# Kernel optimization log

Measured on AMD Instinct MI355X. Metric: run time of the kernel, lower is better.

## Reference

```python
import jax, jax.numpy as jnp
import numpy as np

IDIM, CDIM, NUM_HEADS, N, M = 256, 512, 2, 128, 64
T, BSZ = 64, 128


def setup_inputs() -> dict:
    key = jax.random.key(0)
    ks = jax.random.split(key, 12)
    return {
        "embs": jax.random.normal(ks[0], (T, BSZ, IDIM), jnp.float32),
        "lens": jnp.clip(jax.random.randint(ks[1], (BSZ,), 0, 64), 1, T).astype(jnp.int32),
        "mem_bias": jax.random.normal(ks[2], (N, M), jnp.float32) * 0.05,
        "W_ih": jax.random.normal(ks[3], (4 * CDIM, IDIM + NUM_HEADS * M), jnp.float32) * 0.04,
        "W_hh": jax.random.normal(ks[4], (4 * CDIM, CDIM), jnp.float32) * 0.04,
        "b_ih": jnp.zeros((4 * CDIM,), jnp.float32),
        "b_hh": jnp.zeros((4 * CDIM,), jnp.float32),
        "Wr": jax.random.normal(ks[5], (NUM_HEADS, M + 6, CDIM), jnp.float32) * 0.04,
        "br": jnp.zeros((NUM_HEADS, M + 6), jnp.float32),
        "Ww": jax.random.normal(ks[6], (NUM_HEADS, 3 * M + 6, CDIM), jnp.float32) * 0.04,
        "bw": jnp.zeros((NUM_HEADS, 3 * M + 6), jnp.float32),
        "h0": jax.random.normal(ks[7], (CDIM,), jnp.float32) * 0.05,
        "c0": jax.random.normal(ks[8], (CDIM,), jnp.float32) * 0.05,
        "r0": jax.random.normal(ks[9], (NUM_HEADS, M), jnp.float32) * 0.02,
    }


def _address(mem, k, beta, g, s, gamma, w_prev):
    # mem: (b,N,M)  k:(b,M)  beta,g,gamma:(b,1)  s:(b,3)  w_prev:(b,N)
    beta = jax.nn.softplus(beta)
    g = jax.nn.sigmoid(g)
    s = jax.nn.softmax(s, axis=1)
    gamma = 1.0 + jax.nn.softplus(gamma)
    kk = k + 1e-16
    mm = mem + 1e-16
    dot = jnp.einsum('bnm,bm->bn', mm, kk)
    denom = jnp.linalg.norm(mm, axis=-1) * jnp.linalg.norm(kk, axis=-1, keepdims=True)
    sim = dot / jnp.maximum(denom, 1e-8)  # torch cosine_similarity eps
    wc = jax.nn.softmax(beta * sim, axis=1)
    wg = g * wc + (1.0 - g) * w_prev
    # circular convolution with 3-tap shift kernel: c[i]=s0*w[i-1]+s1*w[i]+s2*w[i+1]
    ww = (s[:, 0:1] * jnp.roll(wg, 1, axis=1)
          + s[:, 1:2] * wg
          + s[:, 2:3] * jnp.roll(wg, -1, axis=1))
    wp = ww ** gamma
    return wp / (jnp.sum(wp, axis=1, keepdims=True) + 1e-16)


def _split5(o):
    return o[:, :M], o[:, M:M + 1], o[:, M + 1:M + 2], o[:, M + 2:M + 5], o[:, M + 5:M + 6]


def _ntm_forward(embs, mem_bias, W_ih, W_hh, b_ih, b_hh, Wr, br, Ww, bw, h0, c0, r0):
    bsz = embs.shape[1]
    mem0 = jnp.broadcast_to(mem_bias, (bsz, N, M))
    reads0 = jnp.broadcast_to(r0[:, None, :], (NUM_HEADS, bsz, M))
    w0 = jnp.zeros((NUM_HEADS, bsz, N), embs.dtype)
    h = jnp.broadcast_to(h0, (bsz, CDIM))
    c = jnp.broadcast_to(c0, (bsz, CDIM))

    def step(carry, emb):
        h, c, mem, rw, wws, reads = carry
        x = jnp.concatenate([emb] + [reads[i] for i in range(NUM_HEADS)], axis=1)
        gates = x @ W_ih.T + h @ W_hh.T + (b_ih + b_hh)
        gi, gf, gg, go = jnp.split(gates, 4, axis=1)  # torch LSTM gate order i,f,g,o
        c = jax.nn.sigmoid(gf) * c + jax.nn.sigmoid(gi) * jnp.tanh(gg)
        h = jax.nn.sigmoid(go) * jnp.tanh(c)
        ctrl = h
        new_reads, new_rw, new_wws = [], [], []
        for hi in range(NUM_HEADS):  # head order: read_i then write_i, writes visible to later heads
            orh = ctrl @ Wr[hi].T + br[hi]
            k, beta, g, s, gamma = _split5(orh)
            w = _address(mem, k, beta, g, s, gamma, rw[hi])
            new_rw.append(w)
            new_reads.append(jnp.einsum('bn,bnm->bm', w, mem))
            owh = ctrl @ Ww[hi].T + bw[hi]
            k2, beta2, g2, s2, gamma2 = _split5(owh)
            e = jax.nn.sigmoid(owh[:, M + 6:2 * M + 6])
            a = owh[:, 2 * M + 6:3 * M + 6]
            w2 = _address(mem, k2, beta2, g2, s2, gamma2, wws[hi])
            mem = mem * (1.0 - w2[:, :, None] * e[:, None, :]) + w2[:, :, None] * a[:, None, :]
            new_wws.append(w2)
        o = jnp.concatenate([ctrl] + new_reads, axis=1)
        carry = (h, c, mem, jnp.stack(new_rw), jnp.stack(new_wws), jnp.stack(new_reads))
        return carry, (o, h, c)

    _, (os_, hs, cs) = jax.lax.scan(step, (h, c, mem0, w0, w0, reads0), embs)
    return os_, hs, cs  # (T,b,cdim+H*M), (T,b,cdim), (T,b,cdim)


def reference(embs, lens, mem_bias, W_ih, W_hh, b_ih, b_hh, Wr, br, Ww, bw, h0, c0, r0):
    os_, hs, cs = _ntm_forward(embs, mem_bias, W_ih, W_hh, b_ih, b_hh, Wr, br, Ww, bw, h0, c0, r0)
    bsz = embs.shape[1]
    bi = jnp.arange(bsz)
    h_fin = hs[lens - 1, bi][None]  # (1,b,cdim) final state at true sequence end
    c_fin = cs[lens - 1, bi][None]
    return os_, h_fin, c_fin
```

## Files before the change

kernel.cpp:

```cpp
#include <hip/hip_runtime.h>
#include <cmath>

#define WS_EMBT  0
#define WS_STATE 2097152
#define WS_C     2179072
#define WS_MEM   2244608
#define WS_RW    3293184
#define WS_WWS   3325952
#define WS_PART  3358720

#define GATES_LDS_BYTES ((3584 + 14336) * 4)

__device__ __forceinline__ float sigm(float x) { return 1.0f / (1.0f + expf(-x)); }
__device__ __forceinline__ float softplusf(float x) {
    return fmaxf(x, 0.0f) + log1pf(expf(-fabsf(x)));
}

__global__ __launch_bounds__(256) void k_embT(const float* __restrict__ embs,
                                              float* __restrict__ ws)
{
    int f4 = blockIdx.x * 256 + threadIdx.x;
    int k4 = f4 & 63, b = (f4 >> 6) & 127, t = f4 >> 13;
    float4 v = *(const float4*)&embs[(size_t)(t * 128 + b) * 256 + k4 * 4];
    *(float4*)&ws[WS_EMBT + ((size_t)(t * 64 + k4) * 128 + b) * 4] = v;
}

__global__ __launch_bounds__(256) void k_init(float* __restrict__ ws,
                                              const float* __restrict__ mem_bias,
                                              const float* __restrict__ h0,
                                              const float* __restrict__ c0,
                                              const float* __restrict__ r0)
{
    int i = blockIdx.x * 256 + threadIdx.x;
    if (i < 81920) {
        int ks = i >> 9, rem = i & 511, c4 = rem & 3;
        int k = ks * 4 + c4;
        ws[WS_STATE + i] = (ks < 32) ? r0[k] : h0[k - 128];
        return;
    }
    int j = i - 81920;
    if (j < 65536) { ws[WS_C + j] = c0[j >> 7]; return; }
    j -= 65536;
    if (j < 1048576) { ws[WS_MEM + j] = mem_bias[j & 8191]; return; }
    j -= 1048576;
    ws[WS_RW + j] = 0.0f;
}

__global__ void __launch_bounds__(256, 2) k_gates(
    const float* __restrict__ W_ih,
    const float* __restrict__ W_hh,
    const float* __restrict__ ws_c,
    float* __restrict__ partials,
    int t)
{
    extern __shared__ float sm[];
    float4* w_s4 = (float4*)sm;
    float4* x_s4 = (float4*)(sm + 3584);

    const int tx = threadIdx.x;
    const int rt = blockIdx.x >> 3, kz = blockIdx.x & 7;
    const int r0g = rt * 32, k0 = kz * 112;

#pragma unroll
    for (int it = 0; it < 4; ++it) {
        int f = it * 256 + tx;
        if (f < 896) {
            int rl = f / 28, kq = f - rl * 28;
            int kg = k0 + kq * 4, r = r0g + rl;
            float4 v = (kg < 384) ? *(const float4*)&W_ih[r * 384 + kg]
                                  : *(const float4*)&W_hh[r * 512 + (kg - 384)];
            w_s4[f] = v;
        }
    }
    const float* embsT  = ws_c + WS_EMBT + (size_t)t * 32768;
    const float* stateT = ws_c + WS_STATE;
#pragma unroll
    for (int it = 0; it < 14; ++it) {
        int f = it * 256 + tx;
        int k4 = f >> 7, b = f & 127;
        int k4g = kz * 28 + k4;
        const float* src = (k4g < 64) ? &embsT[(size_t)k4g * 512 + b * 4]
                                      : &stateT[(size_t)(k4g - 64) * 512 + b * 4];
        x_s4[f] = *(const float4*)src;
    }
    __syncthreads();

    const int lane = tx & 63, wid = tx >> 6;
    const int wr0 = wid * 8;
    float acc0[8] = {}, acc1[8] = {};
#pragma unroll 4
    for (int k4 = 0; k4 < 28; ++k4) {
        float4 xv0 = x_s4[k4 * 128 + lane];
        float4 xv1 = x_s4[k4 * 128 + 64 + lane];
#pragma unroll
        for (int r = 0; r < 8; ++r) {
            float4 wv = w_s4[(wr0 + r) * 28 + k4];
            acc0[r] += wv.x * xv0.x + wv.y * xv0.y + wv.z * xv0.z + wv.w * xv0.w;
            acc1[r] += wv.x * xv1.x + wv.y * xv1.y + wv.z * xv1.z + wv.w * xv1.w;
        }
    }
#pragma unroll
    for (int r = 0; r < 8; ++r) {
        int row = r0g + wr0 + r;
        partials[(size_t)kz * 262144 + row * 128 + lane]      = acc0[r];
        partials[(size_t)kz * 262144 + row * 128 + 64 + lane] = acc1[r];
    }
}

__global__ __launch_bounds__(256) void k_lstm(
    const float* __restrict__ partials,
    const float* __restrict__ b_ih,
    const float* __restrict__ b_hh,
    float* __restrict__ ws,
    float* __restrict__ d_out,
    const int* __restrict__ lens,
    int t)
{
    const int tx = threadIdx.x;
    const int half = blockIdx.x & 1, cht = blockIdx.x >> 1;
    const int ch = cht * 4 + (tx >> 6);
    const int lane = tx & 63, b = half * 64 + lane;

    float g4[4];
#pragma unroll
    for (int g = 0; g < 4; ++g) {
        int r = g * 512 + ch;
        float s = b_ih[r] + b_hh[r];
#pragma unroll
        for (int kzq = 0; kzq < 8; ++kzq)
            s += partials[(size_t)kzq * 262144 + r * 128 + b];
        g4[g] = s;
    }
    float* cp = ws + WS_C + ch * 128;
    float c_old = cp[b];
    float c_new = sigm(g4[1]) * c_old + sigm(g4[0]) * tanhf(g4[2]);
    float h_new = sigm(g4[3]) * tanhf(c_new);
    cp[b] = c_new;
    ws[WS_STATE + (32 + (ch >> 2)) * 512 + b * 4 + (ch & 3)] = h_new;
    d_out[((size_t)t * 128 + b) * 640 + ch] = h_new;
    if (lens[b] - 1 == t) {
        d_out[5242880 + b * 512 + ch] = h_new;
        d_out[5308416 + b * 512 + ch] = c_new;
    }
}

__global__ __launch_bounds__(256) void k_proj(
    const float* __restrict__ ws_c,
    const float* __restrict__ Wr,
    const float* __restrict__ Ww,
    float* __restrict__ part2)
{
    __shared__ float w_s[16 * 64];
    __shared__ float x_s[16 * 128 * 4];
    float4* w_s4 = (float4*)w_s;
    float4* x_s4 = (float4*)x_s;

    const int tx = threadIdx.x;
    const int jt = blockIdx.x >> 3, kz = blockIdx.x & 7;
    const int j0 = jt * 16, k0 = kz * 64;
    const float* stateT = ws_c + WS_STATE;

    {
        int rl = tx >> 4, kq = tx & 15;
        int j = j0 + rl;
        float4 v = make_float4(0.f, 0.f, 0.f, 0.f);
        if (j < 536) {
            int hi = j >= 268, q = j - hi * 268;
            v = (q < 70) ? *(const float4*)&Wr[(hi * 70 + q) * 512 + k0 + kq * 4]
                         : *(const float4*)&Ww[(hi * 198 + (q - 70)) * 512 + k0 + kq * 4];
        }
        w_s4[tx] = v;
    }
#pragma unroll
    for (int it = 0; it < 8; ++it) {
        int f = it * 256 + tx;
        int k4 = f >> 7, b = f & 127;
        x_s4[f] = *(const float4*)&stateT[(size_t)(32 + kz * 16 + k4) * 512 + b * 4];
    }
    __syncthreads();

    const int lane = tx & 63, wid = tx >> 6;
    const int jw0 = wid * 4;
    float acc0[4] = {}, acc1[4] = {};
#pragma unroll 4
    for (int k4 = 0; k4 < 16; ++k4) {
        float4 xv0 = x_s4[k4 * 128 + lane];
        float4 xv1 = x_s4[k4 * 128 + 64 + lane];
#pragma unroll
        for (int r = 0; r < 4; ++r) {
            float4 wv = w_s4[(jw0 + r) * 16 + k4];
            acc0[r] += wv.x * xv0.x + wv.y * xv0.y + wv.z * xv0.z + wv.w * xv0.w;
            acc1[r] += wv.x * xv1.x + wv.y * xv1.y + wv.z * xv1.z + wv.w * xv1.w;
        }
    }
#pragma unroll
    for (int r = 0; r < 4; ++r) {
        int j = j0 + jw0 + r;
        if (j < 536) {
            part2[(size_t)kz * 69632 + lane * 544 + j]        = acc0[r];
            part2[(size_t)kz * 69632 + (lane + 64) * 544 + j] = acc1[r];
        }
    }
}

__global__ __launch_bounds__(256) void k_memops(
    const float* __restrict__ part2,
    const float* __restrict__ br,
    const float* __restrict__ bw,
    float* __restrict__ ws,
    float* __restrict__ d_out,
    int t)
{
    const int b = blockIdx.x;
    const int tx = threadIdx.x;
    const int lx = tx & 127;
    const int grp = tx >> 7;
    const int wid = tx >> 6;

    __shared__ float mem_s[128 * 66];
    __shared__ float proj_s[544];
    __shared__ float wg2_s[2 * 128];
    __shared__ float wf_s[2 * 128];
    __shared__ float red_s[16];
    __shared__ float ea_s[128];
    __shared__ float rvp_s[4 * 66];

    float* memg   = ws + WS_MEM;
    float* stateT = ws + WS_STATE;
    float* rwg    = ws + WS_RW;
    float* wwsg   = ws + WS_WWS;

    for (int j = tx; j < 536; j += 256) {
        int hi = j >= 268, q = j - hi * 268;
        float s = (q < 70) ? br[hi * 70 + q] : bw[hi * 198 + (q - 70)];
#pragma unroll
        for (int kzq = 0; kzq < 8; ++kzq)
            s += part2[(size_t)kzq * 69632 + b * 544 + j];
        proj_s[j] = s;
    }
#pragma unroll
    for (int e = 0; e < 8; ++e) {
        int f4 = e * 256 + tx;
        int n = f4 >> 4, m4 = (f4 & 15) * 4;
        float4 v = *(const float4*)&memg[b * 8192 + f4 * 4];
        *(float2*)&mem_s[n * 66 + m4]     = make_float2(v.x, v.y);
        *(float2*)&mem_s[n * 66 + m4 + 2] = make_float2(v.z, v.w);
    }
    __syncthreads();

    for (int hi = 0; hi < 2; ++hi) {
        const float* p = proj_s + hi * 268 + grp * 70;
        float* wprev_g = (grp == 0 ? rwg : wwsg) + (hi * 128 + b) * 128;

        float beta = softplusf(p[64]);
        float g = sigm(p[65]);
        float s0 = p[66], s1 = p[67], s2 = p[68];
        float sm = fmaxf(s0, fmaxf(s1, s2));
        float e0 = expf(s0 - sm), e1 = expf(s1 - sm), e2 = expf(s2 - sm);
        float sden = e0 + e1 + e2;
        s0 = e0 / sden; s1 = e1 / sden; s2 = e2 / sden;
        float gamma = 1.0f + softplusf(p[69]);

        const float* mrow = mem_s + lx * 66;
        float dot = 0.f, nm = 0.f, nk = 0.f;
#pragma unroll
        for (int m = 0; m < 64; m += 2) {
            float2 kv2 = *(const float2*)&p[m];
            float2 mv2 = *(const float2*)&mrow[m];
            float kx = kv2.x + 1e-16f, ky = kv2.y + 1e-16f;
            float mx = mv2.x + 1e-16f, my = mv2.y + 1e-16f;
            dot += mx * kx + my * ky;
            nm  += mx * mx + my * my;
            nk  += kx * kx + ky * ky;
        }
        float sim = dot / fmaxf(sqrtf(nm) * sqrtf(nk), 1e-8f);
        float z = beta * sim;

        float r = z;
#pragma unroll
        for (int d = 32; d > 0; d >>= 1) r = fmaxf(r, __shfl_xor(r, d));
        if ((tx & 63) == 0) red_s[wid] = r;
        __syncthreads();
        float zmax = fmaxf(red_s[grp * 2], red_s[grp * 2 + 1]);
        float ez = expf(z - zmax);
        r = ez;
#pragma unroll
        for (int d = 32; d > 0; d >>= 1) r += __shfl_xor(r, d);
        if ((tx & 63) == 0) red_s[8 + wid] = r;
        __syncthreads();
        float zsum = red_s[8 + grp * 2] + red_s[8 + grp * 2 + 1];
        float wc = ez / zsum;
        float wgv = g * wc + (1.f - g) * wprev_g[lx];
        wg2_s[grp * 128 + lx] = wgv;
        __syncthreads();
        float wwv = s0 * wg2_s[grp * 128 + ((lx + 127) & 127)] + s1 * wgv
                  + s2 * wg2_s[grp * 128 + ((lx + 1) & 127)];
        float wp = powf(wwv, gamma);
        r = wp;
#pragma unroll
        for (int d = 32; d > 0; d >>= 1) r += __shfl_xor(r, d);
        if ((tx & 63) == 0) red_s[wid] = r;
        __syncthreads();
        float psum = red_s[grp * 2] + red_s[grp * 2 + 1];
        float wfin = wp / (psum + 1e-16f);
        wf_s[grp * 128 + lx] = wfin;
        wprev_g[lx] = wfin;
        __syncthreads();

        {
            int m = tx & 63, p4 = tx >> 6;
            float rv = 0.f;
            const int nb = p4 * 32;
#pragma unroll
            for (int n8 = 0; n8 < 32; ++n8) {
                int n = nb + n8;
                rv += wf_s[n] * mem_s[n * 66 + m];
            }
            rvp_s[p4 * 66 + m] = rv;
        }
        if (tx < 64)        ea_s[tx] = sigm(proj_s[hi * 268 + 140 + tx]);
        else if (tx < 128)  ea_s[tx] = proj_s[hi * 268 + 204 + (tx - 64)];
        __syncthreads();

        if (tx < 64) {
            float rvf = rvp_s[tx] + rvp_s[66 + tx] + rvp_s[132 + tx] + rvp_s[198 + tx];
            stateT[((hi * 64 + tx) >> 2) * 512 + b * 4 + (tx & 3)] = rvf;
            d_out[((size_t)t * 128 + b) * 640 + 512 + hi * 64 + tx] = rvf;
        }
#pragma unroll
        for (int e = 0; e < 16; ++e) {
            int f = e * 256 + tx;
            int n = f >> 5, m2 = (f & 31) * 2;
            float w2 = wf_s[128 + n];
            float2 mv = *(const float2*)&mem_s[n * 66 + m2];
            mv.x = mv.x * (1.f - w2 * ea_s[m2])     + w2 * ea_s[64 + m2];
            mv.y = mv.y * (1.f - w2 * ea_s[m2 + 1]) + w2 * ea_s[65 + m2];
            *(float2*)&mem_s[n * 66 + m2] = mv;
            if (hi == 1) *(float2*)&memg[b * 8192 + f * 2] = mv;
        }
        __syncthreads();
    }
}

extern "C" void kernel_launch(void* const* d_in, const int* in_sizes, int n_in,
                              void* d_out, int out_size, void* d_ws, size_t ws_size,
                              hipStream_t stream)
{
    (void)in_sizes; (void)n_in; (void)out_size; (void)ws_size;
    const float* embs     = (const float*)d_in[0];
    const int*   lens     = (const int*)  d_in[1];
    const float* mem_bias = (const float*)d_in[2];
    const float* W_ih     = (const float*)d_in[3];
    const float* W_hh     = (const float*)d_in[4];
    const float* b_ih     = (const float*)d_in[5];
    const float* b_hh     = (const float*)d_in[6];
    const float* Wr       = (const float*)d_in[7];
    const float* br       = (const float*)d_in[8];
    const float* Ww       = (const float*)d_in[9];
    const float* bw       = (const float*)d_in[10];
    const float* h0       = (const float*)d_in[11];
    const float* c0       = (const float*)d_in[12];
    const float* r0       = (const float*)d_in[13];
    float* out = (float*)d_out;
    float* ws  = (float*)d_ws;
    float* partials = ws + WS_PART;
    float* part2    = ws + WS_PART;

    hipFuncSetAttribute(reinterpret_cast<const void*>(&k_gates),
                        hipFuncAttributeMaxDynamicSharedMemorySize, GATES_LDS_BYTES);

    k_embT<<<2048, 256, 0, stream>>>(embs, ws);
    k_init<<<4928, 256, 0, stream>>>(ws, mem_bias, h0, c0, r0);
    for (int t = 0; t < 64; ++t) {
        k_gates<<<512, 256, GATES_LDS_BYTES, stream>>>(W_ih, W_hh, ws, partials, t);
        k_lstm<<<256, 256, 0, stream>>>(partials, b_ih, b_hh, ws, out, lens, t);
        k_proj<<<272, 256, 0, stream>>>(ws, Wr, Ww, part2);
        k_memops<<<128, 256, 0, stream>>>(part2, br, bw, ws, out, t);
    }
}
```

Measured before the change: 2.852 ms.

## Fuse LSTM gate GEMM with cell update and double-buffer hidden state

Merges the split-K gate matmul and the LSTM pointwise kernel into one kernel. Each block computes all four gates for 4 channels over the full K, using double-buffered LDS chunks with register prefetch. This removes the 8-way partials buffer round-trip through global memory and one launch per timestep. The state buffer is ping-ponged by timestep parity so the fused kernel can write the new h without racing blocks that are still reading the old h. The cost is fewer blocks (256 instead of 512) doing longer serial K loops, and a large LDS footprint per block.

```diff
diff --git a/kernel.cpp b/kernel.cpp
--- a/kernel.cpp
+++ b/kernel.cpp
@@ -3,13 +3,14 @@
 
 #define WS_EMBT  0
 #define WS_STATE 2097152
-#define WS_C     2179072
-#define WS_MEM   2244608
-#define WS_RW    3293184
-#define WS_WWS   3325952
-#define WS_PART  3358720
-
-#define GATES_LDS_BYTES ((3584 + 14336) * 4)
+#define WS_C     2260992
+#define WS_MEM   2326528
+#define WS_RW    3375104
+#define WS_WWS   3407872
+#define WS_PART  3440640
+
+#define KA_LDS_FLOATS (14400 + 14336 + 1024 + 16)
+#define KA_LDS_BYTES  (KA_LDS_FLOATS * 4)
 
 __device__ __forceinline__ float sigm(float x) { return 1.0f / (1.0f + expf(-x)); }
 __device__ __forceinline__ float softplusf(float x) {
@@ -33,82 +34,22 @@
 {
     int i = blockIdx.x * 256 + threadIdx.x;
     if (i < 81920) {
-        int ks = i >> 9, rem = i & 511, c4 = rem & 3;
+        int ks = i >> 9, c4 = i & 3;
         int k = ks * 4 + c4;
         ws[WS_STATE + i] = (ks < 32) ? r0[k] : h0[k - 128];
         return;
     }
     int j = i - 81920;
-    if (j < 65536) { ws[WS_C + j] = c0[j >> 7]; return; }
+    if (j < 65536) { ws[WS_C + j] = c0[j & 511]; return; }
     j -= 65536;
     if (j < 1048576) { ws[WS_MEM + j] = mem_bias[j & 8191]; return; }
     j -= 1048576;
     ws[WS_RW + j] = 0.0f;
 }
 
-__global__ void __launch_bounds__(256, 2) k_gates(
+__global__ void __launch_bounds__(512, 1) k_gates_lstm(
     const float* __restrict__ W_ih,
     const float* __restrict__ W_hh,
-    const float* __restrict__ ws_c,
-    float* __restrict__ partials,
-    int t)
-{
-    extern __shared__ float sm[];
-    float4* w_s4 = (float4*)sm;
-    float4* x_s4 = (float4*)(sm + 3584);
-
-    const int tx = threadIdx.x;
-    const int rt = blockIdx.x >> 3, kz = blockIdx.x & 7;
-    const int r0g = rt * 32, k0 = kz * 112;
-
-#pragma unroll
-    for (int it = 0; it < 4; ++it) {
-        int f = it * 256 + tx;
-        if (f < 896) {
-            int rl = f / 28, kq = f - rl * 28;
-            int kg = k0 + kq * 4, r = r0g + rl;
-            float4 v = (kg < 384) ? *(const float4*)&W_ih[r * 384 + kg]
-                                  : *(const float4*)&W_hh[r * 512 + (kg - 384)];
-            w_s4[f] = v;
-        }
-    }
-    const float* embsT  = ws_c + WS_EMBT + (size_t)t * 32768;
-    const float* stateT = ws_c + WS_STATE;
-#pragma unroll
-    for (int it = 0; it < 14; ++it) {
-        int f = it * 256 + tx;
-        int k4 = f >> 7, b = f & 127;
-        int k4g = kz * 28 + k4;
-        const float* src = (k4g < 64) ? &embsT[(size_t)k4g * 512 + b * 4]
-                                      : &stateT[(size_t)(k4g - 64) * 512 + b * 4];
-        x_s4[f] = *(const float4*)src;
-    }
-    __syncthreads();
-
-    const int lane = tx & 63, wid = tx >> 6;
-    const int wr0 = wid * 8;
-    float acc0[8] = {}, acc1[8] = {};
-#pragma unroll 4
-    for (int k4 = 0; k4 < 28; ++k4) {
-        float4 xv0 = x_s4[k4 * 128 + lane];
-        float4 xv1 = x_s4[k4 * 128 + 64 + lane];
-#pragma unroll
-        for (int r = 0; r < 8; ++r) {
-            float4 wv = w_s4[(wr0 + r) * 28 + k4];
-            acc0[r] += wv.x * xv0.x + wv.y * xv0.y + wv.z * xv0.z + wv.w * xv0.w;
-            acc1[r] += wv.x * xv1.x + wv.y * xv1.y + wv.z * xv1.z + wv.w * xv1.w;
-        }
-    }
-#pragma unroll
-    for (int r = 0; r < 8; ++r) {
-        int row = r0g + wr0 + r;
-        partials[(size_t)kz * 262144 + row * 128 + lane]      = acc0[r];
-        partials[(size_t)kz * 262144 + row * 128 + 64 + lane] = acc1[r];
-    }
-}
-
-__global__ __launch_bounds__(256) void k_lstm(
-    const float* __restrict__ partials,
     const float* __restrict__ b_ih,
     const float* __restrict__ b_hh,
     float* __restrict__ ws,
@@ -116,31 +57,112 @@
     const int* __restrict__ lens,
     int t)
 {
+    extern __shared__ float sm[];
+    float4* w_s4 = (float4*)sm;
+    float4* x_s4 = (float4*)(sm + 14400);
+    float*  gx   = sm + 28736;
+    float*  bias = sm + 29760;
+
     const int tx = threadIdx.x;
-    const int half = blockIdx.x & 1, cht = blockIdx.x >> 1;
-    const int ch = cht * 4 + (tx >> 6);
-    const int lane = tx & 63, b = half * 64 + lane;
-
-    float g4[4];
-#pragma unroll
-    for (int g = 0; g < 4; ++g) {
-        int r = g * 512 + ch;
-        float s = b_ih[r] + b_hh[r];
-#pragma unroll
-        for (int kzq = 0; kzq < 8; ++kzq)
-            s += partials[(size_t)kzq * 262144 + r * 128 + b];
-        g4[g] = s;
-    }
-    float* cp = ws + WS_C + ch * 128;
-    float c_old = cp[b];
-    float c_new = sigm(g4[1]) * c_old + sigm(g4[0]) * tanhf(g4[2]);
-    float h_new = sigm(g4[3]) * tanhf(c_new);
-    cp[b] = c_new;
-    ws[WS_STATE + (32 + (ch >> 2)) * 512 + b * 4 + (ch & 3)] = h_new;
-    d_out[((size_t)t * 128 + b) * 640 + ch] = h_new;
-    if (lens[b] - 1 == t) {
-        d_out[5242880 + b * 512 + ch] = h_new;
-        d_out[5308416 + b * 512 + ch] = c_new;
+    const int ct = blockIdx.x >> 1, half = blockIdx.x & 1;
+    const int ch0 = ct * 4;
+    const int p0 = t & 1, p1 = (t + 1) & 1;
+
+#pragma unroll
+    for (int i = 0; i < 7; ++i) {
+        int f = i * 512 + tx;
+        int lr = f / 224, k4 = f - lr * 224;
+        int grow = (lr & 3) * 512 + ch0 + (lr >> 2);
+        int kg = k4 * 4;
+        float4 v = (kg < 384) ? *(const float4*)&W_ih[grow * 384 + kg]
+                              : *(const float4*)&W_hh[grow * 512 + kg - 384];
+        w_s4[lr * 225 + k4] = v;
+    }
+    if (tx < 16) {
+        int grow = (tx & 3) * 512 + ch0 + (tx >> 2);
+        bias[tx] = b_ih[grow] + b_hh[grow];
+    }
+
+    const float* embsT  = ws + WS_EMBT + (size_t)t * 32768;
+    const float* stateT = ws + WS_STATE + (size_t)p0 * 81920;
+
+    float4 pf[4];
+    auto ldchunk = [&](int c) {
+#pragma unroll
+        for (int i = 0; i < 4; ++i) {
+            int f = i * 512 + tx;
+            if (f < 1792) {
+                int k4g = c * 28 + (f >> 6);
+                int b   = half * 64 + (f & 63);
+                pf[i] = (k4g < 64)
+                    ? *(const float4*)&embsT[(size_t)k4g * 512 + b * 4]
+                    : *(const float4*)&stateT[(size_t)(k4g - 64) * 512 + b * 4];
+            }
+        }
+    };
+    auto stchunk = [&](int buf) {
+#pragma unroll
+        for (int i = 0; i < 4; ++i) {
+            int f = i * 512 + tx;
+            if (f < 1792) x_s4[buf * 1792 + f] = pf[i];
+        }
+    };
+
+    ldchunk(0);
+    stchunk(0);
+    __syncthreads();
+
+    const int lane = tx & 63, wid = tx >> 6;
+    const int wr = wid >> 2, wb = wid & 3;
+    const int rl = lane >> 4, bl = lane & 15;
+    const int ra = wr * 8 + rl * 2;
+    const int xoff = wb * 16 + bl;
+
+    const float4* wa  = w_s4 + ra * 225;
+    const float4* wbp = w_s4 + (ra + 1) * 225;
+
+    float acc0 = 0.f, acc1 = 0.f;
+    int cur = 0;
+    for (int c = 0; c < 8; ++c) {
+        if (c < 7) ldchunk(c + 1);
+        const float4* xb = x_s4 + cur * 1792;
+#pragma unroll
+        for (int k4 = 0; k4 < 28; ++k4) {
+            float4 xv = xb[k4 * 64 + xoff];
+            float4 w0 = wa[c * 28 + k4];
+            float4 w1 = wbp[c * 28 + k4];
+            acc0 += w0.x * xv.x + w0.y * xv.y + w0.z * xv.z + w0.w * xv.w;
+            acc1 += w1.x * xv.x + w1.y * xv.y + w1.z * xv.z + w1.w * xv.w;
+        }
+        if (c < 7) {
+            stchunk(cur ^ 1);
+            __syncthreads();
+            cur ^= 1;
+        }
+    }
+
+    gx[ra * 64 + xoff]       = acc0;
+    gx[(ra + 1) * 64 + xoff] = acc1;
+    __syncthreads();
+    if (tx < 256) {
+        int ch_l = tx & 3, b_loc = tx >> 2;
+        int b = half * 64 + b_loc;
+        int ch = ch0 + ch_l;
+        float gi = gx[(ch_l * 4 + 0) * 64 + b_loc] + bias[ch_l * 4 + 0];
+        float gf = gx[(ch_l * 4 + 1) * 64 + b_loc] + bias[ch_l * 4 + 1];
+        float gg = gx[(ch_l * 4 + 2) * 64 + b_loc] + bias[ch_l * 4 + 2];
+        float go = gx[(ch_l * 4 + 3) * 64 + b_loc] + bias[ch_l * 4 + 3];
+        float* cp = ws + WS_C + b * 512 + ch;
+        float c_old = *cp;
+        float c_new = sigm(gf) * c_old + sigm(gi) * tanhf(gg);
+        float h_new = sigm(go) * tanhf(c_new);
+        *cp = c_new;
+        ws[WS_STATE + (size_t)p1 * 81920 + (32 + ct) * 512 + b * 4 + ch_l] = h_new;
+        d_out[((size_t)t * 128 + b) * 640 + ch] = h_new;
+        if (lens[b] - 1 == t) {
+            d_out[5242880 + b * 512 + ch] = h_new;
+            d_out[5308416 + b * 512 + ch] = c_new;
+        }
     }
 }
 
@@ -148,7 +170,8 @@
     const float* __restrict__ ws_c,
     const float* __restrict__ Wr,
     const float* __restrict__ Ww,
-    float* __restrict__ part2)
+    float* __restrict__ part2,
+    int t)
 {
     __shared__ float w_s[16 * 64];
     __shared__ float x_s[16 * 128 * 4];
@@ -158,7 +181,7 @@
     const int tx = threadIdx.x;
     const int jt = blockIdx.x >> 3, kz = blockIdx.x & 7;
     const int j0 = jt * 16, k0 = kz * 64;
-    const float* stateT = ws_c + WS_STATE;
+    const float* stateT = ws_c + WS_STATE + (size_t)((t + 1) & 1) * 81920;
 
     {
         int rl = tx >> 4, kq = tx & 15;
@@ -226,7 +249,7 @@
     __shared__ float rvp_s[4 * 66];
 
     float* memg   = ws + WS_MEM;
-    float* stateT = ws + WS_STATE;
+    float* stateT = ws + WS_STATE + (size_t)((t + 1) & 1) * 81920;
     float* rwg    = ws + WS_RW;
     float* wwsg   = ws + WS_WWS;
 
@@ -363,18 +386,17 @@
     const float* r0       = (const float*)d_in[13];
     float* out = (float*)d_out;
     float* ws  = (float*)d_ws;
-    float* partials = ws + WS_PART;
-    float* part2    = ws + WS_PART;
-
-    hipFuncSetAttribute(reinterpret_cast<const void*>(&k_gates),
-                        hipFuncAttributeMaxDynamicSharedMemorySize, GATES_LDS_BYTES);
+    float* part2 = ws + WS_PART;
+
+    hipFuncSetAttribute(reinterpret_cast<const void*>(&k_gates_lstm),
+                        hipFuncAttributeMaxDynamicSharedMemorySize, KA_LDS_BYTES);
 
     k_embT<<<2048, 256, 0, stream>>>(embs, ws);
     k_init<<<4928, 256, 0, stream>>>(ws, mem_bias, h0, c0, r0);
     for (int t = 0; t < 64; ++t) {
-        k_gates<<<512, 256, GATES_LDS_BYTES, stream>>>(W_ih, W_hh, ws, partials, t);
-        k_lstm<<<256, 256, 0, stream>>>(partials, b_ih, b_hh, ws, out, lens, t);
-        k_proj<<<272, 256, 0, stream>>>(ws, Wr, Ww, part2);
+        k_gates_lstm<<<256, 512, KA_LDS_BYTES, stream>>>(W_ih, W_hh, b_ih, b_hh,
+                                                         ws, out, lens, t);
+        k_proj<<<272, 256, 0, stream>>>(ws, Wr, Ww, part2, t);
         k_memops<<<128, 256, 0, stream>>>(part2, br, bw, ws, out, t);
     }
 }
```

After: 10.88 ms. 282% more time.
